# Performance work log

Measured on AMD Instinct MI355X. Metric: run time of the kernel, lower is better.

The kernel has to match this reference:

```python
import jax, jax.numpy as jnp
import numpy as np

B, T, C = 4, 2048, 2048
H, D = 16, 128  # n_heads, head_dim


def _rope_freqs(seq_len, head_dim, base=10000.0):
    half = head_dim // 2
    inv = 1.0 / (base ** (np.arange(half, dtype=np.float32) / half))
    t = np.arange(seq_len, dtype=np.float32)
    ang = np.outer(t, inv)  # (T, D/2)
    return jnp.asarray(np.stack([np.cos(ang), np.sin(ang)], axis=-1))  # (T, D/2, 2)


def setup_inputs() -> dict:
    key = jax.random.key(0)
    k1, k2, k3 = jax.random.split(key, 3)
    x = jax.random.normal(k1, (B, T, C), dtype=jnp.float32)
    freqs = _rope_freqs(T, D)
    # additive causal mask
    mask = jnp.where(jnp.tril(jnp.ones((T, T), dtype=bool)), 0.0, -1e9).astype(jnp.float32)
    w_qkv = jax.random.normal(k2, (3 * C, C), dtype=jnp.float32) * (1.0 / np.sqrt(C))
    w_out = jax.random.normal(k3, (C, C), dtype=jnp.float32) * (1.0 / np.sqrt(C))
    return {"x": x, "freqs": freqs, "mask": mask, "w_qkv": w_qkv, "w_out": w_out}


def apply_rope(x, freqs):
    # x: (B,H,T,D), freqs: (T,D/2,2)
    xr = x.reshape(*x.shape[:-1], -1, 2)
    cos, sin = freqs[..., 0], freqs[..., 1]
    x0, x1 = xr[..., 0], xr[..., 1]
    rot = jnp.stack([x0 * cos - x1 * sin, x0 * sin + x1 * cos], axis=-1)
    return rot.reshape(x.shape)


def reference(x, freqs, mask, w_qkv, w_out):
    b, t, c = x.shape
    qkv = jnp.einsum('btc,fc->btf', x, w_qkv).reshape(b, t, 3, H, D)
    q, k, v = jnp.moveaxis(qkv, 2, 0)          # each (b,t,H,D)
    q = jnp.transpose(q, (0, 2, 1, 3))          # (b,H,t,D)
    k = jnp.transpose(k, (0, 2, 1, 3))
    v = jnp.transpose(v, (0, 2, 1, 3))
    q = apply_rope(q, freqs[:t])
    k = apply_rope(k, freqs[:t])
    scale = 1.0 / np.sqrt(D).astype(np.float32)
    attn = jnp.einsum('bhqd,bhkd->bhqk', q, k) * scale + mask[:t, :t]
    attn = jax.nn.softmax(attn, axis=-1)
    out = jnp.einsum('bhqk,bhkd->bhqd', attn, v)
    out = jnp.transpose(out, (0, 2, 1, 3)).reshape(b, t, c)
    return jnp.einsum('btc,fc->btf', out, w_out)
```

## Files before the change

### kernel.cpp

```cpp
#include <hip/hip_runtime.h>

typedef unsigned short u16;
typedef unsigned int   u32;

using sx8   = __attribute__((ext_vector_type(8))) short;
using f32x4 = __attribute__((ext_vector_type(4))) float;
using u16x8 = __attribute__((ext_vector_type(8))) unsigned short;

#define BB 4
#define TT 2048
#define CC 2048
#define HH 16
#define DD 128
#define FF 6144
#define MM 8192

static __device__ __forceinline__ u16 f2bf(float f) {
    u32 u = __builtin_bit_cast(u32, f);
    u32 lsb = (u >> 16) & 1u;
    u += 0x7fffu + lsb;
    return (u16)(u >> 16);
}
static __device__ __forceinline__ float bf2f(u16 b) {
    return __builtin_bit_cast(float, (u32)b << 16);
}
static __device__ __forceinline__ f32x4 mfma16(sx8 a, sx8 b, f32x4 c) {
    return __builtin_amdgcn_mfma_f32_16x16x32_bf16(a, b, c, 0, 0, 0);
}

__global__ __launch_bounds__(256) void k_cvt(const float* __restrict__ src,
                                             u16* __restrict__ dst, int n8) {
    int i = blockIdx.x * 256 + threadIdx.x;
    if (i >= n8) return;
    const float4* s = (const float4*)src;
    float4 a = s[2 * (size_t)i], b = s[2 * (size_t)i + 1];
    u16x8 r;
    r[0] = f2bf(a.x); r[1] = f2bf(a.y); r[2] = f2bf(a.z); r[3] = f2bf(a.w);
    r[4] = f2bf(b.x); r[5] = f2bf(b.y); r[6] = f2bf(b.z); r[7] = f2bf(b.w);
    *(u16x8*)(dst + 8 * (size_t)i) = r;
}

template <int OUTF32>
__global__ __launch_bounds__(256, 2) void k_gemm(const u16* __restrict__ A,
                                                 const u16* __restrict__ Bt,
                                                 float* __restrict__ Cf,
                                                 u16* __restrict__ Cb,
                                                 int M, int N, int K) {
    __shared__ __align__(16) u16 sA[128 * 32];
    __shared__ __align__(16) u16 sB[128 * 32];
    const int n0 = blockIdx.x * 128, m0 = blockIdx.y * 128;
    const int tid = threadIdx.x, w = tid >> 6, l = tid & 63;
    const int wm = w >> 1, wn = w & 1;
    const int lr = l & 15, lg = l >> 4;
    f32x4 acc[4][4] = {};

    const int idx0 = w * 128 + l;
    const int idx1 = idx0 + 64;
    const int ra0 = idx0 >> 2, ca0 = (idx0 & 3) * 8;
    const int ra1 = idx1 >> 2, ca1 = (idx1 & 3) * 8;
    const u16* Ar0 = A + (size_t)(m0 + ra0) * K + ca0;
    const u16* Ar1 = A + (size_t)(m0 + ra1) * K + ca1;
    const u16* Br0 = Bt + (size_t)(n0 + ra0) * K + ca0;
    const u16* Br1 = Bt + (size_t)(n0 + ra1) * K + ca1;
    u16* sAd0 = sA + (w * 2 + 0) * 512;
    u16* sAd1 = sA + (w * 2 + 1) * 512;
    u16* sBd0 = sB + (w * 2 + 0) * 512;
    u16* sBd1 = sB + (w * 2 + 1) * 512;

    for (int k0 = 0; k0 < K; k0 += 32) {
        __builtin_amdgcn_global_load_lds(
            (const __attribute__((address_space(1))) void*)(Ar0 + k0),
            (__attribute__((address_space(3))) void*)sAd0, 16, 0, 0);
        __builtin_amdgcn_global_load_lds(
            (const __attribute__((address_space(1))) void*)(Ar1 + k0),
            (__attribute__((address_space(3))) void*)sAd1, 16, 0, 0);
        __builtin_amdgcn_global_load_lds(
            (const __attribute__((address_space(1))) void*)(Br0 + k0),
            (__attribute__((address_space(3))) void*)sBd0, 16, 0, 0);
        __builtin_amdgcn_global_load_lds(
            (const __attribute__((address_space(1))) void*)(Br1 + k0),
            (__attribute__((address_space(3))) void*)sBd1, 16, 0, 0);
        __syncthreads();
        sx8 af[4], bfr[4];
#pragma unroll
        for (int i = 0; i < 4; i++)
            af[i] = *(const sx8*)(sA + (wm * 64 + i * 16 + lr) * 32 + lg * 8);
#pragma unroll
        for (int j = 0; j < 4; j++)
            bfr[j] = *(const sx8*)(sB + (wn * 64 + j * 16 + lr) * 32 + lg * 8);
#pragma unroll
        for (int i = 0; i < 4; i++)
#pragma unroll
            for (int j = 0; j < 4; j++)
                acc[i][j] = mfma16(af[i], bfr[j], acc[i][j]);
        __syncthreads();
    }
#pragma unroll
    for (int i = 0; i < 4; i++) {
        const int mr = m0 + wm * 64 + i * 16 + lg * 4;
#pragma unroll
        for (int j = 0; j < 4; j++) {
            const int nc = n0 + wn * 64 + j * 16 + lr;
#pragma unroll
            for (int rg = 0; rg < 4; rg++) {
                float v = acc[i][j][rg];
                size_t off = (size_t)(mr + rg) * N + nc;
                if (OUTF32) Cf[off] = v;
                else        Cb[off] = f2bf(v);
            }
        }
    }
}

__global__ __launch_bounds__(256) void k_rope(const u16* __restrict__ qkv,
                                              const float* __restrict__ freqs,
                                              u16* __restrict__ Qo,
                                              u16* __restrict__ Ko,
                                              u16* __restrict__ Vt) {
    const int t0 = blockIdx.x * 64, h = blockIdx.y, b = blockIdx.z;
    const int tid = threadIdx.x;
    __shared__ u16 vt[64][129];
#pragma unroll
    for (int it = 0; it < 16; ++it) {
        int idx = tid + it * 256;
        int trow = idx >> 6, pr = idx & 63;
        int t = t0 + trow;
        size_t ib = (size_t)(b * TT + t) * FF + h * DD + 2 * pr;
        float2 cs = *(const float2*)(freqs + (size_t)t * DD + 2 * pr);
        size_t ob = ((size_t)(b * HH + h) * TT + t) * DD + 2 * pr;
        {
            u32 qp = *(const u32*)(qkv + ib);
            float x0 = bf2f((u16)(qp & 0xffff)), x1 = bf2f((u16)(qp >> 16));
            u32 r = (u32)f2bf(x0 * cs.x - x1 * cs.y) |
                    ((u32)f2bf(x0 * cs.y + x1 * cs.x) << 16);
            *(u32*)(Qo + ob) = r;
        }
        {
            u32 kp = *(const u32*)(qkv + ib + CC);
            float x0 = bf2f((u16)(kp & 0xffff)), x1 = bf2f((u16)(kp >> 16));
            u32 r = (u32)f2bf(x0 * cs.x - x1 * cs.y) |
                    ((u32)f2bf(x0 * cs.y + x1 * cs.x) << 16);
            *(u32*)(Ko + ob) = r;
        }
        {
            u32 vp = *(const u32*)(qkv + ib + 2 * CC);
            vt[trow][2 * pr]     = (u16)(vp & 0xffff);
            vt[trow][2 * pr + 1] = (u16)(vp >> 16);
        }
    }
    __syncthreads();
    const size_t vb = (size_t)(b * HH + h) * DD * TT + t0;
#pragma unroll
    for (int it = 0; it < 32; ++it) {
        int idx = tid + it * 256;
        int d = idx >> 6, tr = idx & 63;
        Vt[vb + (size_t)d * TT + tr] = vt[tr][d];
    }
}

#define KV 64
#define PST 72

__global__ __launch_bounds__(256, 2) void k_attn(const u16* __restrict__ Q,
                                                 const u16* __restrict__ K,
                                                 const u16* __restrict__ Vt,
                                                 u16* __restrict__ AO) {
    const int fid = blockIdx.x + 8 * blockIdx.y + 128 * blockIdx.z;
    const int xg = fid >> 6;
    const int hb = fid & 63;
    const int h = hb & 15, b = hb >> 4;

    const int tid = threadIdx.x, w = tid >> 6, l = tid & 63;
    const int lr = l & 15, lg = l >> 4;
    const size_t bh = (size_t)(b * HH + h);
    const u16* Qh = Q + bh * TT * DD;
    const u16* Kh = K + bh * TT * DD;
    const u16* Vh = Vt + bh * DD * TT;

    __shared__ __align__(16) u16 sK[2][KV * DD];
    __shared__ __align__(16) u16 sP[4][32 * PST];
    u16* myP = sP[w];

    const int strow = tid >> 4;
    const int sc16  = tid & 15;
    const float scale = 0.08838834764831845f;

    for (int rep = 0; rep < 2; ++rep) {
        const int g = rep ? (15 - xg) : xg;
        const int q0w = g * 128 + w * 32;
        const int nt = 2 * g + 2;

        sx8 qf[2][4];
#pragma unroll
        for (int i = 0; i < 2; i++)
#pragma unroll
            for (int kk = 0; kk < 4; kk++)
                qf[i][kk] = *(const sx8*)(Qh + (size_t)(q0w + i * 16 + lr) * DD + kk * 32 + lg * 8);

        f32x4 o[2][8] = {};
        float mrow[2][4], lrow[2][4];
#pragma unroll
        for (int i = 0; i < 2; i++)
#pragma unroll
            for (int rg = 0; rg < 4; rg++) { mrow[i][rg] = -1e30f; lrow[i][rg] = 0.0f; }

#pragma unroll
        for (int i = 0; i < 4; ++i) {
            const int row = i * 16 + strow;
            const int scol = (sc16 ^ (row & 7)) * 8;
            __builtin_amdgcn_global_load_lds(
                (const __attribute__((address_space(1))) void*)(Kh + (size_t)row * DD + scol),
                (__attribute__((address_space(3))) void*)(&sK[0][i * 2048 + w * 512]),
                16, 0, 0);
        }
        __syncthreads();

        int cur = 0;
        for (int t = 0; t < nt; ++t) {
            const int k0 = t * KV;
            if (t + 1 < nt) {
                const int kn = k0 + KV;
#pragma unroll
                for (int i = 0; i < 4; ++i) {
                    const int row = i * 16 + strow;
                    const int scol = (sc16 ^ (row & 7)) * 8;
                    __builtin_amdgcn_global_load_lds(
                        (const __attribute__((address_space(1))) void*)(Kh + (size_t)(kn + row) * DD + scol),
                        (__attribute__((address_space(3))) void*)(&sK[cur ^ 1][i * 2048 + w * 512]),
                        16, 0, 0);
                }
            }
            if (k0 <= q0w) {
                f32x4 s2[2][4] = {};
#pragma unroll
                for (int j = 0; j < 4; ++j) {
                    const int row = j * 16 + lr;
                    const int rx = row & 7;
#pragma unroll
                    for (int kk = 0; kk < 4; ++kk) {
                        const int c16 = (kk * 4 + lg) ^ rx;
                        sx8 kf = *(const sx8*)(&sK[cur][row * DD + c16 * 8]);
                        s2[0][j] = mfma16(qf[0][kk], kf, s2[0][j]);
                        s2[1][j] = mfma16(qf[1][kk], kf, s2[1][j]);
                    }
                }
                sx8 vf0[8];
#pragma unroll
                for (int n = 0; n < 8; ++n)
                    vf0[n] = *(const sx8*)(Vh + (size_t)(n * 16 + lr) * TT + k0 + lg * 8);

                const bool need_mask = (k0 + 63 > q0w);
#pragma unroll
                for (int i = 0; i < 2; ++i) {
#pragma unroll
                    for (int rg = 0; rg < 4; ++rg) {
                        const int rloc = i * 16 + lg * 4 + rg;
                        float a0 = s2[i][0][rg] * scale, a1 = s2[i][1][rg] * scale;
                        float a2 = s2[i][2][rg] * scale, a3 = s2[i][3][rg] * scale;
                        if (need_mask) {
                            const int cl = q0w + rloc - k0;
                            if (lr      > cl) a0 = -1e30f;
                            if (16 + lr > cl) a1 = -1e30f;
                            if (32 + lr > cl) a2 = -1e30f;
                            if (48 + lr > cl) a3 = -1e30f;
                        }
                        float pm = fmaxf(fmaxf(a0, a1), fmaxf(a2, a3));
#pragma unroll
                        for (int d2 = 1; d2 < 16; d2 <<= 1) pm = fmaxf(pm, __shfl_xor(pm, d2));
                        const float mold = mrow[i][rg];
                        const float mnew = fmaxf(mold, pm);
                        const float sf = __expf(mold - mnew);
                        mrow[i][rg] = mnew;
                        float p0 = __expf(a0 - mnew), p1 = __expf(a1 - mnew);
                        float p2 = __expf(a2 - mnew), p3 = __expf(a3 - mnew);
                        float rs = (p0 + p1) + (p2 + p3);
#pragma unroll
                        for (int d2 = 1; d2 < 16; d2 <<= 1) rs += __shfl_xor(rs, d2);
                        lrow[i][rg] = lrow[i][rg] * sf + rs;
#pragma unroll
                        for (int n = 0; n < 8; ++n) o[i][n][rg] *= sf;
                        myP[rloc * PST + lr]      = f2bf(p0);
                        myP[rloc * PST + 16 + lr] = f2bf(p1);
                        myP[rloc * PST + 32 + lr] = f2bf(p2);
                        myP[rloc * PST + 48 + lr] = f2bf(p3);
                    }
                }
                asm volatile("s_waitcnt lgkmcnt(0)" ::: "memory");
                __builtin_amdgcn_sched_barrier(0);

                sx8 pa0[2], pa1[2];
                pa0[0] = *(const sx8*)(myP + (size_t)lr * PST + lg * 8);
                pa0[1] = *(const sx8*)(myP + (size_t)(16 + lr) * PST + lg * 8);
                pa1[0] = *(const sx8*)(myP + (size_t)lr * PST + 32 + lg * 8);
                pa1[1] = *(const sx8*)(myP + (size_t)(16 + lr) * PST + 32 + lg * 8);
#pragma unroll
                for (int n = 0; n < 8; ++n) {
                    o[0][n] = mfma16(pa0[0], vf0[n], o[0][n]);
                    o[1][n] = mfma16(pa0[1], vf0[n], o[1][n]);
                }
#pragma unroll
                for (int n = 0; n < 8; ++n) {
                    sx8 vf1 = *(const sx8*)(Vh + (size_t)(n * 16 + lr) * TT + k0 + 32 + lg * 8);
                    o[0][n] = mfma16(pa1[0], vf1, o[0][n]);
                    o[1][n] = mfma16(pa1[1], vf1, o[1][n]);
                }
            }
            __syncthreads();
            cur ^= 1;
        }

#pragma unroll
        for (int i = 0; i < 2; ++i) {
#pragma unroll
            for (int rg = 0; rg < 4; ++rg) {
                const float inv = 1.0f / lrow[i][rg];
                const int tq = q0w + i * 16 + lg * 4 + rg;
                u16* orow = AO + ((size_t)(b * TT) + tq) * CC + h * DD + lr;
#pragma unroll
                for (int n = 0; n < 8; ++n)
                    orow[n * 16] = f2bf(o[i][n][rg] * inv);
            }
        }
    }
}

extern "C" void kernel_launch(void* const* d_in, const int* in_sizes, int n_in,
                              void* d_out, int out_size, void* d_ws, size_t ws_size,
                              hipStream_t stream) {
    const float* x     = (const float*)d_in[0];
    const float* freqs = (const float*)d_in[1];
    const float* w_qkv = (const float*)d_in[3];
    const float* w_out = (const float*)d_in[4];
    float* out = (float*)d_out;

    u16* ws   = (u16*)d_ws;
    u16* xb   = ws;
    u16* wqb  = xb   + (size_t)MM * CC;
    u16* wob  = wqb  + (size_t)FF * CC;
    u16* qkvb = wob  + (size_t)CC * CC;
    u16* Qr   = qkvb + (size_t)MM * FF;
    u16* Kr   = Qr   + (size_t)MM * CC;
    u16* Vt   = Kr   + (size_t)MM * CC;
    u16* AO   = qkvb;

    k_cvt<<<MM * CC / 2048, 256, 0, stream>>>(x, xb, MM * CC / 8);
    k_cvt<<<FF * CC / 2048, 256, 0, stream>>>(w_qkv, wqb, FF * CC / 8);
    k_cvt<<<CC * CC / 2048, 256, 0, stream>>>(w_out, wob, CC * CC / 8);

    k_gemm<0><<<dim3(FF / 128, MM / 128), 256, 0, stream>>>(xb, wqb, nullptr, qkvb, MM, FF, CC);
    k_rope<<<dim3(TT / 64, HH, BB), 256, 0, stream>>>(qkvb, freqs, Qr, Kr, Vt);
    k_attn<<<dim3(8, HH, BB), 256, 0, stream>>>(Qr, Kr, Vt, AO);
    k_gemm<1><<<dim3(CC / 128, MM / 128), 256, 0, stream>>>(AO, wob, out, nullptr, MM, CC, CC);
}
```

Baseline: 584.0 us.

## Drop shared K staging, load K per-warp from global, add lazy softmax rescale

Removes the block-wide double-buffered K tile in LDS and the per-tile __syncthreads. Each warp now reads K fragments directly from global memory and runs only its own causal tile count. It also adds a lazy online-softmax rescale that updates the running max only when the new max exceeds the old by more than 8, skipping the O rescale otherwise. Launch bounds rise to 4 blocks per CU and the P stride shrinks, aiming for higher occupancy and less barrier stalling, at the cost of redundant K global traffic across warps and higher register pressure.

```diff
diff --git a/kernel.cpp b/kernel.cpp
--- a/kernel.cpp
+++ b/kernel.cpp
@@ -159,9 +159,9 @@
 }
 
 #define KV 64
-#define PST 72
-
-__global__ __launch_bounds__(256, 2) void k_attn(const u16* __restrict__ Q,
+#define PST 68
+
+__global__ __launch_bounds__(256, 4) void k_attn(const u16* __restrict__ Q,
                                                  const u16* __restrict__ K,
                                                  const u16* __restrict__ Vt,
                                                  u16* __restrict__ AO) {
@@ -177,18 +177,14 @@
     const u16* Kh = K + bh * TT * DD;
     const u16* Vh = Vt + bh * DD * TT;
 
-    __shared__ __align__(16) u16 sK[2][KV * DD];
     __shared__ __align__(16) u16 sP[4][32 * PST];
     u16* myP = sP[w];
-
-    const int strow = tid >> 4;
-    const int sc16  = tid & 15;
     const float scale = 0.08838834764831845f;
 
     for (int rep = 0; rep < 2; ++rep) {
         const int g = rep ? (15 - xg) : xg;
         const int q0w = g * 128 + w * 32;
-        const int nt = 2 * g + 2;
+        const int ntw = (q0w >> 6) + 1;
 
         sx8 qf[2][4];
 #pragma unroll
@@ -204,109 +200,88 @@
 #pragma unroll
             for (int rg = 0; rg < 4; rg++) { mrow[i][rg] = -1e30f; lrow[i][rg] = 0.0f; }
 
-#pragma unroll
-        for (int i = 0; i < 4; ++i) {
-            const int row = i * 16 + strow;
-            const int scol = (sc16 ^ (row & 7)) * 8;
-            __builtin_amdgcn_global_load_lds(
-                (const __attribute__((address_space(1))) void*)(Kh + (size_t)row * DD + scol),
-                (__attribute__((address_space(3))) void*)(&sK[0][i * 2048 + w * 512]),
-                16, 0, 0);
-        }
-        __syncthreads();
-
-        int cur = 0;
-        for (int t = 0; t < nt; ++t) {
+        for (int t = 0; t < ntw; ++t) {
             const int k0 = t * KV;
-            if (t + 1 < nt) {
-                const int kn = k0 + KV;
-#pragma unroll
-                for (int i = 0; i < 4; ++i) {
-                    const int row = i * 16 + strow;
-                    const int scol = (sc16 ^ (row & 7)) * 8;
-                    __builtin_amdgcn_global_load_lds(
-                        (const __attribute__((address_space(1))) void*)(Kh + (size_t)(kn + row) * DD + scol),
-                        (__attribute__((address_space(3))) void*)(&sK[cur ^ 1][i * 2048 + w * 512]),
-                        16, 0, 0);
+            f32x4 s2[2][4] = {};
+#pragma unroll
+            for (int j = 0; j < 4; ++j) {
+                sx8 kf[4];
+#pragma unroll
+                for (int kk = 0; kk < 4; ++kk)
+                    kf[kk] = *(const sx8*)(Kh + (size_t)(k0 + j * 16 + lr) * DD + kk * 32 + lg * 8);
+#pragma unroll
+                for (int kk = 0; kk < 4; ++kk) {
+                    s2[0][j] = mfma16(qf[0][kk], kf[kk], s2[0][j]);
+                    s2[1][j] = mfma16(qf[1][kk], kf[kk], s2[1][j]);
                 }
             }
-            if (k0 <= q0w) {
-                f32x4 s2[2][4] = {};
-#pragma unroll
-                for (int j = 0; j < 4; ++j) {
-                    const int row = j * 16 + lr;
-                    const int rx = row & 7;
-#pragma unroll
-                    for (int kk = 0; kk < 4; ++kk) {
-                        const int c16 = (kk * 4 + lg) ^ rx;
-                        sx8 kf = *(const sx8*)(&sK[cur][row * DD + c16 * 8]);
-                        s2[0][j] = mfma16(qf[0][kk], kf, s2[0][j]);
-                        s2[1][j] = mfma16(qf[1][kk], kf, s2[1][j]);
+            sx8 vf0[8];
+#pragma unroll
+            for (int n = 0; n < 8; ++n)
+                vf0[n] = *(const sx8*)(Vh + (size_t)(n * 16 + lr) * TT + k0 + lg * 8);
+
+            const bool need_mask = (t == ntw - 1);
+#pragma unroll
+            for (int i = 0; i < 2; ++i) {
+                f32x4 sfv;
+                int anyresc = 0;
+#pragma unroll
+                for (int rg = 0; rg < 4; ++rg) {
+                    const int rloc = i * 16 + lg * 4 + rg;
+                    float a0 = s2[i][0][rg] * scale, a1 = s2[i][1][rg] * scale;
+                    float a2 = s2[i][2][rg] * scale, a3 = s2[i][3][rg] * scale;
+                    if (need_mask) {
+                        const int cl = q0w + rloc - k0;
+                        if (lr      > cl) a0 = -1e30f;
+                        if (16 + lr > cl) a1 = -1e30f;
+                        if (32 + lr > cl) a2 = -1e30f;
+                        if (48 + lr > cl) a3 = -1e30f;
                     }
+                    float pm = fmaxf(fmaxf(a0, a1), fmaxf(a2, a3));
+#pragma unroll
+                    for (int d2 = 1; d2 < 16; d2 <<= 1) pm = fmaxf(pm, __shfl_xor(pm, d2));
+                    const float mold = mrow[i][rg];
+                    const bool resc = pm > mold + 8.0f;
+                    const float mnew = resc ? pm : mold;
+                    mrow[i][rg] = mnew;
+                    float p0 = __expf(a0 - mnew), p1 = __expf(a1 - mnew);
+                    float p2 = __expf(a2 - mnew), p3 = __expf(a3 - mnew);
+                    float rs = (p0 + p1) + (p2 + p3);
+#pragma unroll
+                    for (int d2 = 1; d2 < 16; d2 <<= 1) rs += __shfl_xor(rs, d2);
+                    const float sf = resc ? __expf(mold - mnew) : 1.0f;
+                    lrow[i][rg] = lrow[i][rg] * sf + rs;
+                    sfv[rg] = sf;
+                    anyresc |= (int)resc;
+                    myP[rloc * PST + lr]      = f2bf(p0);
+                    myP[rloc * PST + 16 + lr] = f2bf(p1);
+                    myP[rloc * PST + 32 + lr] = f2bf(p2);
+                    myP[rloc * PST + 48 + lr] = f2bf(p3);
                 }
-                sx8 vf0[8];
-#pragma unroll
-                for (int n = 0; n < 8; ++n)
-                    vf0[n] = *(const sx8*)(Vh + (size_t)(n * 16 + lr) * TT + k0 + lg * 8);
-
-                const bool need_mask = (k0 + 63 > q0w);
-#pragma unroll
-                for (int i = 0; i < 2; ++i) {
-#pragma unroll
-                    for (int rg = 0; rg < 4; ++rg) {
-                        const int rloc = i * 16 + lg * 4 + rg;
-                        float a0 = s2[i][0][rg] * scale, a1 = s2[i][1][rg] * scale;
-                        float a2 = s2[i][2][rg] * scale, a3 = s2[i][3][rg] * scale;
-                        if (need_mask) {
-                            const int cl = q0w + rloc - k0;
-                            if (lr      > cl) a0 = -1e30f;
-                            if (16 + lr > cl) a1 = -1e30f;
-                            if (32 + lr > cl) a2 = -1e30f;
-                            if (48 + lr > cl) a3 = -1e30f;
-                        }
-                        float pm = fmaxf(fmaxf(a0, a1), fmaxf(a2, a3));
-#pragma unroll
-                        for (int d2 = 1; d2 < 16; d2 <<= 1) pm = fmaxf(pm, __shfl_xor(pm, d2));
-                        const float mold = mrow[i][rg];
-                        const float mnew = fmaxf(mold, pm);
-                        const float sf = __expf(mold - mnew);
-                        mrow[i][rg] = mnew;
-                        float p0 = __expf(a0 - mnew), p1 = __expf(a1 - mnew);
-                        float p2 = __expf(a2 - mnew), p3 = __expf(a3 - mnew);
-                        float rs = (p0 + p1) + (p2 + p3);
-#pragma unroll
-                        for (int d2 = 1; d2 < 16; d2 <<= 1) rs += __shfl_xor(rs, d2);
-                        lrow[i][rg] = lrow[i][rg] * sf + rs;
-#pragma unroll
-                        for (int n = 0; n < 8; ++n) o[i][n][rg] *= sf;
-                        myP[rloc * PST + lr]      = f2bf(p0);
-                        myP[rloc * PST + 16 + lr] = f2bf(p1);
-                        myP[rloc * PST + 32 + lr] = f2bf(p2);
-                        myP[rloc * PST + 48 + lr] = f2bf(p3);
-                    }
+                if (anyresc) {
+#pragma unroll
+                    for (int n = 0; n < 8; ++n) o[i][n] *= sfv;
                 }
-                asm volatile("s_waitcnt lgkmcnt(0)" ::: "memory");
-                __builtin_amdgcn_sched_barrier(0);
-
-                sx8 pa0[2], pa1[2];
-                pa0[0] = *(const sx8*)(myP + (size_t)lr * PST + lg * 8);
-                pa0[1] = *(const sx8*)(myP + (size_t)(16 + lr) * PST + lg * 8);
-                pa1[0] = *(const sx8*)(myP + (size_t)lr * PST + 32 + lg * 8);
-                pa1[1] = *(const sx8*)(myP + (size_t)(16 + lr) * PST + 32 + lg * 8);
-#pragma unroll
-                for (int n = 0; n < 8; ++n) {
-                    o[0][n] = mfma16(pa0[0], vf0[n], o[0][n]);
-                    o[1][n] = mfma16(pa0[1], vf0[n], o[1][n]);
-                }
-#pragma unroll
-                for (int n = 0; n < 8; ++n) {
-                    sx8 vf1 = *(const sx8*)(Vh + (size_t)(n * 16 + lr) * TT + k0 + 32 + lg * 8);
-                    o[0][n] = mfma16(pa1[0], vf1, o[0][n]);
-                    o[1][n] = mfma16(pa1[1], vf1, o[1][n]);
-                }
-            }
-            __syncthreads();
-            cur ^= 1;
+            }
+            asm volatile("s_waitcnt lgkmcnt(0)" ::: "memory");
+            __builtin_amdgcn_sched_barrier(0);
+
+            sx8 pa0[2], pa1[2];
+            pa0[0] = *(const sx8*)(myP + (size_t)lr * PST + lg * 8);
+            pa0[1] = *(const sx8*)(myP + (size_t)(16 + lr) * PST + lg * 8);
+            pa1[0] = *(const sx8*)(myP + (size_t)lr * PST + 32 + lg * 8);
+            pa1[1] = *(const sx8*)(myP + (size_t)(16 + lr) * PST + 32 + lg * 8);
+#pragma unroll
+            for (int n = 0; n < 8; ++n) {
+                o[0][n] = mfma16(pa0[0], vf0[n], o[0][n]);
+                o[1][n] = mfma16(pa0[1], vf0[n], o[1][n]);
+            }
+#pragma unroll
+            for (int n = 0; n < 8; ++n) {
+                sx8 vf1 = *(const sx8*)(Vh + (size_t)(n * 16 + lr) * TT + k0 + 32 + lg * 8);
+                o[0][n] = mfma16(pa1[0], vf1, o[0][n]);
+                o[1][n] = mfma16(pa1[1], vf1, o[1][n]);
+            }
         }
 
 #pragma unroll
```

Result: slower. 1.245 ms (+113.2%).

## Transpose score MFMA, fold softmax scale into Q, lazily rescale online softmax

Applied to the files above, without the earlier changes.

Computes S^T by swapping MFMA operands so each lane holds one query row's scores across registers. This replaces the 16-lane shuffle reductions with two shuffles and lets P be written as packed 64-bit stores. The softmax scale is folded into Q during RoPE, which removes per-score multiplies. Output and row-sum rescaling is skipped unless the running max grows by more than 8, cutting exp and multiply work. The exchange is a P layout and padding change (PST 68) that may bring LDS bank conflicts, and the lazy-max threshold adds some numerical risk.

```diff
diff --git a/kernel.cpp b/kernel.cpp
--- a/kernel.cpp
+++ b/kernel.cpp
@@ -26,6 +26,9 @@
 }
 static __device__ __forceinline__ f32x4 mfma16(sx8 a, sx8 b, f32x4 c) {
     return __builtin_amdgcn_mfma_f32_16x16x32_bf16(a, b, c, 0, 0, 0);
+}
+static __device__ __forceinline__ u32 pkbf(float a, float b) {
+    return (u32)f2bf(a) | ((u32)f2bf(b) << 16);
 }
 
 __global__ __launch_bounds__(256) void k_cvt(const float* __restrict__ src,
@@ -119,6 +122,7 @@
                                               u16* __restrict__ Vt) {
     const int t0 = blockIdx.x * 64, h = blockIdx.y, b = blockIdx.z;
     const int tid = threadIdx.x;
+    const float scale = 0.08838834764831845f;
     __shared__ u16 vt[64][129];
 #pragma unroll
     for (int it = 0; it < 16; ++it) {
@@ -131,8 +135,8 @@
         {
             u32 qp = *(const u32*)(qkv + ib);
             float x0 = bf2f((u16)(qp & 0xffff)), x1 = bf2f((u16)(qp >> 16));
-            u32 r = (u32)f2bf(x0 * cs.x - x1 * cs.y) |
-                    ((u32)f2bf(x0 * cs.y + x1 * cs.x) << 16);
+            u32 r = (u32)f2bf((x0 * cs.x - x1 * cs.y) * scale) |
+                    ((u32)f2bf((x0 * cs.y + x1 * cs.x) * scale) << 16);
             *(u32*)(Qo + ob) = r;
         }
         {
@@ -159,7 +163,7 @@
 }
 
 #define KV 64
-#define PST 72
+#define PST 68
 
 __global__ __launch_bounds__(256, 2) void k_attn(const u16* __restrict__ Q,
                                                  const u16* __restrict__ K,
@@ -183,7 +187,6 @@
 
     const int strow = tid >> 4;
     const int sc16  = tid & 15;
-    const float scale = 0.08838834764831845f;
 
     for (int rep = 0; rep < 2; ++rep) {
         const int g = rep ? (15 - xg) : xg;
@@ -198,11 +201,8 @@
                 qf[i][kk] = *(const sx8*)(Qh + (size_t)(q0w + i * 16 + lr) * DD + kk * 32 + lg * 8);
 
         f32x4 o[2][8] = {};
-        float mrow[2][4], lrow[2][4];
-#pragma unroll
-        for (int i = 0; i < 2; i++)
-#pragma unroll
-            for (int rg = 0; rg < 4; rg++) { mrow[i][rg] = -1e30f; lrow[i][rg] = 0.0f; }
+        float mrow[2] = {-1e30f, -1e30f};
+        float lrow[2] = {0.0f, 0.0f};
 
 #pragma unroll
         for (int i = 0; i < 4; ++i) {
@@ -231,17 +231,21 @@
                 }
             }
             if (k0 <= q0w) {
-                f32x4 s2[2][4] = {};
+                f32x4 st[2][4] = {};
 #pragma unroll
                 for (int j = 0; j < 4; ++j) {
                     const int row = j * 16 + lr;
                     const int rx = row & 7;
+                    sx8 kf[4];
 #pragma unroll
                     for (int kk = 0; kk < 4; ++kk) {
                         const int c16 = (kk * 4 + lg) ^ rx;
-                        sx8 kf = *(const sx8*)(&sK[cur][row * DD + c16 * 8]);
-                        s2[0][j] = mfma16(qf[0][kk], kf, s2[0][j]);
-                        s2[1][j] = mfma16(qf[1][kk], kf, s2[1][j]);
+                        kf[kk] = *(const sx8*)(&sK[cur][row * DD + c16 * 8]);
+                    }
+#pragma unroll
+                    for (int kk = 0; kk < 4; ++kk) {
+                        st[0][j] = mfma16(kf[kk], qf[0][kk], st[0][j]);
+                        st[1][j] = mfma16(kf[kk], qf[1][kk], st[1][j]);
                     }
                 }
                 sx8 vf0[8];
@@ -250,39 +254,51 @@
                     vf0[n] = *(const sx8*)(Vh + (size_t)(n * 16 + lr) * TT + k0 + lg * 8);
 
                 const bool need_mask = (k0 + 63 > q0w);
+                const int klocal = lg * 4;
 #pragma unroll
                 for (int i = 0; i < 2; ++i) {
-#pragma unroll
-                    for (int rg = 0; rg < 4; ++rg) {
-                        const int rloc = i * 16 + lg * 4 + rg;
-                        float a0 = s2[i][0][rg] * scale, a1 = s2[i][1][rg] * scale;
-                        float a2 = s2[i][2][rg] * scale, a3 = s2[i][3][rg] * scale;
-                        if (need_mask) {
-                            const int cl = q0w + rloc - k0;
-                            if (lr      > cl) a0 = -1e30f;
-                            if (16 + lr > cl) a1 = -1e30f;
-                            if (32 + lr > cl) a2 = -1e30f;
-                            if (48 + lr > cl) a3 = -1e30f;
-                        }
-                        float pm = fmaxf(fmaxf(a0, a1), fmaxf(a2, a3));
-#pragma unroll
-                        for (int d2 = 1; d2 < 16; d2 <<= 1) pm = fmaxf(pm, __shfl_xor(pm, d2));
-                        const float mold = mrow[i][rg];
-                        const float mnew = fmaxf(mold, pm);
-                        const float sf = __expf(mold - mnew);
-                        mrow[i][rg] = mnew;
-                        float p0 = __expf(a0 - mnew), p1 = __expf(a1 - mnew);
-                        float p2 = __expf(a2 - mnew), p3 = __expf(a3 - mnew);
-                        float rs = (p0 + p1) + (p2 + p3);
-#pragma unroll
-                        for (int d2 = 1; d2 < 16; d2 <<= 1) rs += __shfl_xor(rs, d2);
-                        lrow[i][rg] = lrow[i][rg] * sf + rs;
-#pragma unroll
-                        for (int n = 0; n < 8; ++n) o[i][n][rg] *= sf;
-                        myP[rloc * PST + lr]      = f2bf(p0);
-                        myP[rloc * PST + 16 + lr] = f2bf(p1);
-                        myP[rloc * PST + 32 + lr] = f2bf(p2);
-                        myP[rloc * PST + 48 + lr] = f2bf(p3);
+                    if (need_mask) {
+                        const int cl = q0w + i * 16 + lr - k0;
+#pragma unroll
+                        for (int j = 0; j < 4; ++j)
+#pragma unroll
+                            for (int rg = 0; rg < 4; ++rg)
+                                if (j * 16 + klocal + rg > cl) st[i][j][rg] = -1e30f;
+                    }
+                    f32x4 m4;
+#pragma unroll
+                    for (int rg = 0; rg < 4; ++rg)
+                        m4[rg] = fmaxf(fmaxf(st[i][0][rg], st[i][1][rg]),
+                                       fmaxf(st[i][2][rg], st[i][3][rg]));
+                    float pm = fmaxf(fmaxf(m4[0], m4[1]), fmaxf(m4[2], m4[3]));
+                    pm = fmaxf(pm, __shfl_xor(pm, 16));
+                    pm = fmaxf(pm, __shfl_xor(pm, 32));
+                    const float mold = mrow[i];
+                    const bool resc = pm > mold + 8.0f;
+                    const float mnew = resc ? pm : mold;
+                    mrow[i] = mnew;
+                    float rs = 0.0f;
+#pragma unroll
+                    for (int j = 0; j < 4; ++j) {
+                        float p0 = __expf(st[i][j][0] - mnew);
+                        float p1 = __expf(st[i][j][1] - mnew);
+                        float p2 = __expf(st[i][j][2] - mnew);
+                        float p3 = __expf(st[i][j][3] - mnew);
+                        rs += (p0 + p1) + (p2 + p3);
+                        *(uint2*)(myP + (i * 16 + lr) * PST + j * 16 + klocal) =
+                            make_uint2(pkbf(p0, p1), pkbf(p2, p3));
+                    }
+                    rs += __shfl_xor(rs, 16);
+                    rs += __shfl_xor(rs, 32);
+                    const float sf = resc ? __expf(mold - mnew) : 1.0f;
+                    lrow[i] = lrow[i] * sf + rs;
+                    if (__any(resc)) {
+                        f32x4 sfo;
+#pragma unroll
+                        for (int rg = 0; rg < 4; ++rg)
+                            sfo[rg] = __shfl(sf, 4 * lg + rg);
+#pragma unroll
+                        for (int n = 0; n < 8; ++n) o[i][n] *= sfo;
                     }
                 }
                 asm volatile("s_waitcnt lgkmcnt(0)" ::: "memory");
@@ -311,9 +327,13 @@
 
 #pragma unroll
         for (int i = 0; i < 2; ++i) {
+            f32x4 linv;
+#pragma unroll
+            for (int rg = 0; rg < 4; ++rg)
+                linv[rg] = __shfl(lrow[i], 4 * lg + rg);
 #pragma unroll
             for (int rg = 0; rg < 4; ++rg) {
-                const float inv = 1.0f / lrow[i][rg];
+                const float inv = 1.0f / linv[rg];
                 const int tq = q0w + i * 16 + lg * 4 + rg;
                 u16* orow = AO + ((size_t)(b * TT) + tq) * CC + h * DD + lr;
 #pragma unroll
```

Result: faster. 544.3 us (-6.8%).
